# Performance work log

Measured on AMD Instinct MI355X. Metric: run time of the kernel, lower is better.

## Reference

```python
import jax, jax.numpy as jnp
import numpy as np

N = 4096        # nodes
D = 512         # in_dim = hidden_dim
E = 131072      # edges (avg degree 32)
K = 3           # aggregate_range
ALPHA = 2.0


def prelu(x, a):
    return jnp.where(x >= 0, x, a * x)


def setup_inputs() -> dict:
    key = jax.random.key(0)
    ks = jax.random.split(key, 8)
    s = 1.0 / np.sqrt(D)  # ~xavier scale
    return {
        "coeffs": jax.random.normal(ks[0], (N, D), jnp.float32),
        "edge_index": jax.random.randint(ks[1], (2, E), 0, N, dtype=jnp.int32),
        "W0": jax.random.normal(ks[2], (D, D), jnp.float32) * s,
        "b0": jnp.zeros((D,), jnp.float32),
        "a0": jnp.full((1,), 0.25, jnp.float32),
        "W1": jax.random.normal(ks[3], (D, D), jnp.float32) * s,  # use_bias=False
        "a1": jnp.full((1,), 0.25, jnp.float32),
        "W2": jax.random.normal(ks[4], (D, D), jnp.float32) * s,
        "a2": jnp.full((1,), 0.25, jnp.float32),
        "Wo": jax.random.normal(ks[5], (1, D), jnp.float32) * s,
        "bo": jnp.zeros((1,), jnp.float32),
    }


def _mlp(coeffs, W0, b0, a0, W1, a1, W2, a2, Wo, bo):
    # Linear+PReLU, then n_hidden_layers x [Linear(no bias)+PReLU+(Dropout: eval, no-op)], then Linear
    x = prelu(coeffs @ W0.T + b0, a0)
    x = prelu(x @ W1.T, a1)
    x = prelu(x @ W2.T, a2)
    return x @ Wo.T + bo  # [N, 1]


def _aggregate_k_hop(edge_index, angles):
    # Faithful to the torch code: enhanced_angles aliases angles, so each hop
    # reads the CURRENT (already enhanced) values:  a <- a + w_k * A_k @ a.
    # Hop 1 uses raw edge list (duplicate edges add twice). Hops >= 2 use
    # np.unique-deduplicated composed paths == boolean adjacency powers.
    src, dst = edge_index[0], edge_index[1]
    a = angles
    a = a + (0.5 ** ALPHA) * jax.ops.segment_sum(a[dst], src, num_segments=N)
    A = jnp.zeros((N, N), jnp.float32).at[src, dst].set(1.0)  # dedup'd boolean adjacency
    Ak = A
    for k_ in range(K - 1):
        Ak = ((Ak @ A) > 0).astype(jnp.float32)  # unique k-hop paths
        a = a + (1.0 / (k_ + 3)) ** ALPHA * (Ak @ a)
    return a


def reference(coeffs, edge_index, W0, b0, a0, W1, a1, W2, a2, Wo, bo):
    angles = _mlp(coeffs, W0, b0, a0, W1, a1, W2, a2, Wo, bo)
    return _aggregate_k_hop(edge_index, angles)
```

## Files before the change

kernel.cpp:

```cpp
#include <hip/hip_runtime.h>

#define N_NODES 4096
#define D_DIM   512
#define E_EDGES 131072
#define NWORDS  128
#define MLP_BLOCKS 256

typedef __bf16 bf16;
typedef __bf16 bf16x4 __attribute__((ext_vector_type(4)));
typedef __bf16 bf16x8 __attribute__((ext_vector_type(8)));
typedef float  f32x4  __attribute__((ext_vector_type(4)));
typedef unsigned int u32;

static const size_t OFF_W0P = 0;
static const size_t OFF_W1P = OFF_W0P + (size_t)D_DIM*D_DIM*2;
static const size_t OFF_W2P = OFF_W1P + (size_t)D_DIM*D_DIM*2;
static const size_t OFF_ANG = OFF_W2P + (size_t)D_DIM*D_DIM*2;
static const size_t OFF_H1  = OFF_ANG + N_NODES*4;
static const size_t OFF_A2V = OFF_H1  + N_NODES*4;
static const size_t OFF_TP  = OFF_A2V + N_NODES*4;
static const size_t OFF_AB  = OFF_TP  + 1024*4;
static const size_t OFF_A2B = OFF_AB  + (size_t)N_NODES*NWORDS*4;
static const size_t OFF_A3B = OFF_A2B + (size_t)N_NODES*NWORDS*4;

__device__ __forceinline__ bf16x8 cvt8(float4 lo, float4 hi) {
    bf16x8 r;
    r[0] = (bf16)lo.x; r[1] = (bf16)lo.y; r[2] = (bf16)lo.z; r[3] = (bf16)lo.w;
    r[4] = (bf16)hi.x; r[5] = (bf16)hi.y; r[6] = (bf16)hi.z; r[7] = (bf16)hi.w;
    return r;
}

__global__ __launch_bounds__(256)
void prep(const float* __restrict__ W0, const float* __restrict__ W1,
          const float* __restrict__ W2,
          bf16* __restrict__ W0p, bf16* __restrict__ W1p, bf16* __restrict__ W2p,
          u32* __restrict__ Ab, float* __restrict__ h1)
{
    const int bx = blockIdx.x, t = threadIdx.x;
    if (bx < 192) {
        const int layer = bx >> 6;
        const float* src = (layer == 0) ? W0 : (layer == 1) ? W1 : W2;
        bf16* dst = (layer == 0) ? W0p : (layer == 1) ? W1p : W2p;
        #pragma unroll
        for (int i = 0; i < 2; ++i) {
            int p = (bx & 63) * 512 + i * 256 + t;
            int colblk = p >> 12, ks = (p >> 8) & 15, f = (p >> 6) & 3, lane = p & 63;
            int col = colblk * 64 + f * 16 + (lane & 15);
            int k   = ks * 32 + (lane >> 4) * 8;
            const float* s = src + (size_t)col * D_DIM + k;
            float4 lo = *(const float4*)(s);
            float4 hi = *(const float4*)(s + 4);
            *(bf16x8*)(dst + (size_t)p * 8) = cvt8(lo, hi);
        }
    } else if (bx < 320) {
        uint4* dst = (uint4*)Ab + (size_t)(bx - 192) * 1024;
        uint4 z = {0u, 0u, 0u, 0u};
        #pragma unroll
        for (int i = 0; i < 4; ++i) dst[i * 256 + t] = z;
    } else {
        for (int i = t; i < N_NODES; i += 256) h1[i] = 0.f;
    }
}

__device__ __forceinline__ void gemm16x64(const bf16 (*xin)[512], const bf16* __restrict__ Wp,
                                          int wave, int lane, int lq, int quad, f32x4 acc[4])
{
    #pragma unroll
    for (int ks = 0; ks < 16; ++ks) {
        bf16x8 a = *(const bf16x8*)&xin[lq][(((ks * 4 + quad) ^ (lq & 7)) << 3)];
        #pragma unroll
        for (int f = 0; f < 4; ++f) {
            bf16x8 b = *(const bf16x8*)(Wp + ((size_t)((wave * 16 + ks) * 4 + f) * 64 + lane) * 8);
            acc[f] = __builtin_amdgcn_mfma_f32_16x16x32_bf16(a, b, acc[f], 0, 0, 0);
        }
    }
}

__device__ __forceinline__ void store_act(bf16 (*xout)[512], const f32x4 acc[4],
                                          int col0, int lq, int quad,
                                          const float* __restrict__ bias, float sl)
{
    #pragma unroll
    for (int f = 0; f < 4; ++f) {
        int col = col0 + f * 16 + lq;
        float bv = bias ? bias[col] : 0.f;
        int c = col >> 3, e = col & 7;
        #pragma unroll
        for (int r = 0; r < 4; ++r) {
            int row = quad * 4 + r;
            float v = acc[f][r] + bv;
            v = (v >= 0.f) ? v : sl * v;
            xout[row][((c ^ (row & 7)) << 3) + e] = (bf16)v;
        }
    }
}

__global__ __launch_bounds__(512)
void mlp_fused(const float* __restrict__ coeffs,
               const bf16* __restrict__ W0p, const bf16* __restrict__ W1p,
               const bf16* __restrict__ W2p,
               const float* __restrict__ b0, const float* __restrict__ pa0,
               const float* __restrict__ pa1, const float* __restrict__ pa2,
               const float* __restrict__ Wo, const float* __restrict__ bo,
               float* __restrict__ ang,
               const int* __restrict__ esrc, const int* __restrict__ edst,
               u32* __restrict__ AbOut)
{
    __shared__ bf16 xa[16][512];
    __shared__ bf16 xb[16][512];
    __shared__ float s_ang[8][16];
    const int bx = blockIdx.x, t = threadIdx.x;

    if (bx < MLP_BLOCKS) {
        const int wave = t >> 6, lane = t & 63;
        const int quad = lane >> 4, lq = lane & 15;
        const int rb = bx * 16;
        const int col0 = wave * 64;

        {
            int r = t >> 5;
            int kc = (t & 31) * 16;
            const float* src = coeffs + (size_t)(rb + r) * 512 + kc;
            float4 v0 = *(const float4*)(src);
            float4 v1 = *(const float4*)(src + 4);
            float4 v2 = *(const float4*)(src + 8);
            float4 v3 = *(const float4*)(src + 12);
            int c0 = kc >> 3;
            *(bf16x8*)&xa[r][((c0 ^ (r & 7)) << 3)]       = cvt8(v0, v1);
            *(bf16x8*)&xa[r][(((c0 + 1) ^ (r & 7)) << 3)] = cvt8(v2, v3);
        }
        __syncthreads();

        {
            f32x4 acc[4] = {};
            gemm16x64(xa, W0p, wave, lane, lq, quad, acc);
            store_act(xb, acc, col0, lq, quad, b0, pa0[0]);
        }
        __syncthreads();
        {
            f32x4 acc[4] = {};
            gemm16x64(xb, W1p, wave, lane, lq, quad, acc);
            store_act(xa, acc, col0, lq, quad, nullptr, pa1[0]);
        }
        __syncthreads();
        {
            f32x4 acc[4] = {};
            gemm16x64(xa, W2p, wave, lane, lq, quad, acc);
            const float sl = pa2[0];
            float wo[4];
            #pragma unroll
            for (int f = 0; f < 4; ++f) wo[f] = Wo[col0 + f * 16 + lq];
            #pragma unroll
            for (int r = 0; r < 4; ++r) {
                float p = 0.f;
                #pragma unroll
                for (int f = 0; f < 4; ++f) {
                    float v = acc[f][r];
                    v = (v >= 0.f) ? v : sl * v;
                    p += v * wo[f];
                }
                #pragma unroll
                for (int m = 1; m < 16; m <<= 1) p += __shfl_xor(p, m, 64);
                if (lq == 0) s_ang[wave][quad * 4 + r] = p;
            }
        }
        __syncthreads();
        if (t < 16) {
            float s = bo[0];
            #pragma unroll
            for (int w2 = 0; w2 < 8; ++w2) s += s_ang[w2][t];
            ang[rb + t] = s;
        }
    } else {
        int base = (bx - MLP_BLOCKS) * 512 + t;
        for (int e = base; e < E_EDGES; e += 128 * 512) {
            int r = esrc[e], c = edst[e];
            atomicOr(&AbOut[(size_t)r * NWORDS + (c >> 5)], 1u << (c & 31));
        }
    }
}

__device__ __forceinline__ void row_or(int row, int wave, int lane,
                                       int* s_cnt, int (*s_list)[256],
                                       const u32* __restrict__ P, const u32* __restrict__ Q,
                                       u32* __restrict__ BOut)
{
    if (lane == 0) s_cnt[wave] = 0;
    __syncthreads();
    const u32* prow = P + (size_t)row * NWORDS;
    #pragma unroll
    for (int h = 0; h < 2; ++h) {
        u32 bits = prow[h * 64 + lane];
        int base = (h * 64 + lane) * 32;
        while (bits) {
            int b = __ffs(bits) - 1; bits &= bits - 1;
            int pos = atomicAdd(&s_cnt[wave], 1);
            if (pos < 256) s_list[wave][pos] = base + b;
        }
    }
    __syncthreads();
    int cnt = min(s_cnt[wave], 256);
    u32 acc0 = 0, acc1 = 0;
    int j = 0;
    for (; j + 4 <= cnt; j += 4) {
        int i0 = s_list[wave][j], i1 = s_list[wave][j + 1];
        int i2 = s_list[wave][j + 2], i3 = s_list[wave][j + 3];
        const u32* q0 = Q + (size_t)i0 * NWORDS;
        const u32* q1 = Q + (size_t)i1 * NWORDS;
        const u32* q2 = Q + (size_t)i2 * NWORDS;
        const u32* q3 = Q + (size_t)i3 * NWORDS;
        u32 x0 = q0[lane], x1 = q1[lane], x2 = q2[lane], x3 = q3[lane];
        u32 y0 = q0[64 + lane], y1 = q1[64 + lane], y2 = q2[64 + lane], y3 = q3[64 + lane];
        acc0 |= x0 | x1 | x2 | x3;
        acc1 |= y0 | y1 | y2 | y3;
    }
    for (; j < cnt; ++j) {
        const u32* q = Q + (size_t)s_list[wave][j] * NWORDS;
        acc0 |= q[lane]; acc1 |= q[64 + lane];
    }
    BOut[(size_t)row * NWORDS + lane]      = acc0;
    BOut[(size_t)row * NWORDS + 64 + lane] = acc1;
}

__global__ __launch_bounds__(256)
void hop1_rowor(const int* __restrict__ src, const int* __restrict__ dst,
                const float* __restrict__ ang, float* __restrict__ h1,
                const u32* __restrict__ P, const u32* __restrict__ Q, u32* __restrict__ BOut)
{
    __shared__ int s_cnt[4];
    __shared__ int s_list[4][256];
    const int bx = blockIdx.x, t = threadIdx.x;
    const int wave = t >> 6, lane = t & 63;
    if (bx < 512) {
        int e = bx * 256 + t;
        atomicAdd(&h1[src[e]], 0.25f * ang[dst[e]]);
    } else {
        row_or((bx - 512) * 4 + wave, wave, lane, s_cnt, s_list, P, Q, BOut);
    }
}

__global__ __launch_bounds__(256)
void bmv2_rowor(const u32* __restrict__ A2, const float* __restrict__ ang,
                const float* __restrict__ h1, float* __restrict__ a2,
                float* __restrict__ Tpart,
                const u32* __restrict__ P, const u32* __restrict__ Q, u32* __restrict__ BOut)
{
    __shared__ float aLds[N_NODES];
    __shared__ float s_red[4];
    __shared__ int s_cnt[4];
    __shared__ int s_list[4][256];
    const int bx = blockIdx.x, t = threadIdx.x;
    const int wave = t >> 6, lane = t & 63;

    if (bx < 1024) {
        #pragma unroll
        for (int i = 0; i < 4; ++i) {
            int e = (i * 256 + t) * 4;
            float4 va = *(const float4*)(ang + e);
            float4 vh = *(const float4*)(h1 + e);
            float4 o; o.x = va.x + vh.x; o.y = va.y + vh.y; o.z = va.z + vh.z; o.w = va.w + vh.w;
            *(float4*)(aLds + e) = o;
        }
        __syncthreads();

        int row = bx * 4 + wave;
        float s = 0.f;
        #pragma unroll
        for (int h = 0; h < 2; ++h) {
            u32 bits = A2[(size_t)row * NWORDS + h * 64 + lane];
            int base = (h * 64 + lane) * 32;
            while (bits) {
                int b = __ffs(bits) - 1;
                bits &= bits - 1;
                s += aLds[base + b];
            }
        }
        #pragma unroll
        for (int off = 32; off > 0; off >>= 1) s += __shfl_down(s, off, 64);
        if (lane == 0) {
            float val = aLds[row] + (1.f / 9.f) * s;
            a2[row] = val;
            s_red[wave] = val;
        }
        __syncthreads();
        if (t == 0)
            Tpart[bx] = s_red[0] + s_red[1] + s_red[2] + s_red[3];
    } else {
        row_or((bx - 1024) * 4 + wave, wave, lane, s_cnt, s_list, P, Q, BOut);
    }
}

__global__ __launch_bounds__(256)
void bits_matvec3(const u32* __restrict__ A3, const float* __restrict__ a2,
                  const float* __restrict__ Tpart, float* __restrict__ out)
{
    __shared__ float aLds[N_NODES];
    __shared__ float s_part[4];
    const int t = threadIdx.x, wave = t >> 6, lane = t & 63;

    #pragma unroll
    for (int i = 0; i < 4; ++i) {
        int e = (i * 256 + t) * 4;
        *(float4*)(aLds + e) = *(const float4*)(a2 + e);
    }

    float tsum = 0.f;
    #pragma unroll
    for (int i = 0; i < 4; ++i) tsum += Tpart[i * 256 + t];
    #pragma unroll
    for (int off = 32; off > 0; off >>= 1) tsum += __shfl_down(tsum, off, 64);
    if (lane == 0) s_part[wave] = tsum;
    __syncthreads();
    const float T = s_part[0] + s_part[1] + s_part[2] + s_part[3];

    int row = blockIdx.x * 4 + wave;
    float s = 0.f;
    #pragma unroll
    for (int h = 0; h < 2; ++h) {
        u32 bits = ~A3[(size_t)row * NWORDS + h * 64 + lane];
        int base = (h * 64 + lane) * 32;
        while (bits) {
            int b = __ffs(bits) - 1;
            bits &= bits - 1;
            s += aLds[base + b];
        }
    }
    #pragma unroll
    for (int off = 32; off > 0; off >>= 1) s += __shfl_down(s, off, 64);
    if (lane == 0) out[row] = aLds[row] + (1.f / 16.f) * (T - s);
}

extern "C" void kernel_launch(void* const* d_in, const int* in_sizes, int n_in,
                              void* d_out, int out_size, void* d_ws, size_t ws_size,
                              hipStream_t stream) {
    const float* coeffs = (const float*)d_in[0];
    const int*   edges  = (const int*)d_in[1];
    const float* W0     = (const float*)d_in[2];
    const float* b0     = (const float*)d_in[3];
    const float* pa0    = (const float*)d_in[4];
    const float* W1     = (const float*)d_in[5];
    const float* pa1    = (const float*)d_in[6];
    const float* W2     = (const float*)d_in[7];
    const float* pa2    = (const float*)d_in[8];
    const float* Wo     = (const float*)d_in[9];
    const float* bo     = (const float*)d_in[10];
    float* out = (float*)d_out;

    char* ws = (char*)d_ws;
    bf16*  W0p  = (bf16*)(ws + OFF_W0P);
    bf16*  W1p  = (bf16*)(ws + OFF_W1P);
    bf16*  W2p  = (bf16*)(ws + OFF_W2P);
    float* ang  = (float*)(ws + OFF_ANG);
    float* h1   = (float*)(ws + OFF_H1);
    float* a2v  = (float*)(ws + OFF_A2V);
    float* Tp   = (float*)(ws + OFF_TP);
    u32*   Ab   = (u32*)(ws + OFF_AB);
    u32*   A2b  = (u32*)(ws + OFF_A2B);
    u32*   A3b  = (u32*)(ws + OFF_A3B);

    const int* srcp = edges;
    const int* dstp = edges + E_EDGES;

    prep<<<321, 256, 0, stream>>>(W0, W1, W2, W0p, W1p, W2p, Ab, h1);

    mlp_fused<<<MLP_BLOCKS + 128, 512, 0, stream>>>(coeffs, W0p, W1p, W2p, b0, pa0, pa1, pa2,
                                                    Wo, bo, ang, srcp, dstp, Ab);

    hop1_rowor<<<1536, 256, 0, stream>>>(srcp, dstp, ang, h1, Ab, Ab, A2b);

    bmv2_rowor<<<2048, 256, 0, stream>>>(A2b, ang, h1, a2v, Tp, Ab, A2b, A3b);

    bits_matvec3<<<1024, 256, 0, stream>>>(A3b, a2v, Tp, out);
}
```

Before: 129.7 us.

## Build adjacency bitmap in prep via per-block LDS row-range scans

Adjacency bitmap construction moves out of the MLP kernel's extra blocks into the prep kernel. Each of 128 blocks owns 32 rows, scans the full edge list, and sets bits with LDS atomicOr before one coalesced write to global memory. This removes the global zero-fill and the scattered global atomics, and frees the MLP kernel from sharing the GPU with the edge blocks. The cost is that every block reads all 131072 edge sources, about 128x redundant reads of esrc, which hit in L2 but add per-block loop latency.

After: 267.4 us. +106.2%, slower.

```diff
diff --git a/kernel.cpp b/kernel.cpp
--- a/kernel.cpp
+++ b/kernel.cpp
@@ -34,8 +34,10 @@
 void prep(const float* __restrict__ W0, const float* __restrict__ W1,
           const float* __restrict__ W2,
           bf16* __restrict__ W0p, bf16* __restrict__ W1p, bf16* __restrict__ W2p,
+          const int* __restrict__ esrc, const int* __restrict__ edst,
           u32* __restrict__ Ab, float* __restrict__ h1)
 {
+    __shared__ u32 sAb[32][NWORDS];
     const int bx = blockIdx.x, t = threadIdx.x;
     if (bx < 192) {
         const int layer = bx >> 6;
@@ -53,10 +55,23 @@
             *(bf16x8*)(dst + (size_t)p * 8) = cvt8(lo, hi);
         }
     } else if (bx < 320) {
-        uint4* dst = (uint4*)Ab + (size_t)(bx - 192) * 1024;
-        uint4 z = {0u, 0u, 0u, 0u};
-        #pragma unroll
-        for (int i = 0; i < 4; ++i) dst[i * 256 + t] = z;
+        int r0 = (bx - 192) * 32;
+        #pragma unroll
+        for (int i = 0; i < 16; ++i) ((u32*)sAb)[i * 256 + t] = 0u;
+        __syncthreads();
+        for (int e = t; e < E_EDGES; e += 256) {
+            int r = esrc[e];
+            if ((unsigned)(r - r0) < 32u) {
+                int c = edst[e];
+                atomicOr(&sAb[r - r0][c >> 5], 1u << (c & 31));
+            }
+        }
+        __syncthreads();
+        #pragma unroll
+        for (int i = 0; i < 16; ++i) {
+            int w = i * 256 + t;
+            Ab[(size_t)r0 * NWORDS + w] = ((u32*)sAb)[w];
+        }
     } else {
         for (int i = t; i < N_NODES; i += 256) h1[i] = 0.f;
     }
@@ -102,81 +117,71 @@
                const float* __restrict__ b0, const float* __restrict__ pa0,
                const float* __restrict__ pa1, const float* __restrict__ pa2,
                const float* __restrict__ Wo, const float* __restrict__ bo,
-               float* __restrict__ ang,
-               const int* __restrict__ esrc, const int* __restrict__ edst,
-               u32* __restrict__ AbOut)
+               float* __restrict__ ang)
 {
     __shared__ bf16 xa[16][512];
     __shared__ bf16 xb[16][512];
     __shared__ float s_ang[8][16];
     const int bx = blockIdx.x, t = threadIdx.x;
 
-    if (bx < MLP_BLOCKS) {
-        const int wave = t >> 6, lane = t & 63;
-        const int quad = lane >> 4, lq = lane & 15;
-        const int rb = bx * 16;
-        const int col0 = wave * 64;
-
-        {
-            int r = t >> 5;
-            int kc = (t & 31) * 16;
-            const float* src = coeffs + (size_t)(rb + r) * 512 + kc;
-            float4 v0 = *(const float4*)(src);
-            float4 v1 = *(const float4*)(src + 4);
-            float4 v2 = *(const float4*)(src + 8);
-            float4 v3 = *(const float4*)(src + 12);
-            int c0 = kc >> 3;
-            *(bf16x8*)&xa[r][((c0 ^ (r & 7)) << 3)]       = cvt8(v0, v1);
-            *(bf16x8*)&xa[r][(((c0 + 1) ^ (r & 7)) << 3)] = cvt8(v2, v3);
-        }
-        __syncthreads();
-
-        {
-            f32x4 acc[4] = {};
-            gemm16x64(xa, W0p, wave, lane, lq, quad, acc);
-            store_act(xb, acc, col0, lq, quad, b0, pa0[0]);
-        }
-        __syncthreads();
-        {
-            f32x4 acc[4] = {};
-            gemm16x64(xb, W1p, wave, lane, lq, quad, acc);
-            store_act(xa, acc, col0, lq, quad, nullptr, pa1[0]);
-        }
-        __syncthreads();
-        {
-            f32x4 acc[4] = {};
-            gemm16x64(xa, W2p, wave, lane, lq, quad, acc);
-            const float sl = pa2[0];
-            float wo[4];
+    const int wave = t >> 6, lane = t & 63;
+    const int quad = lane >> 4, lq = lane & 15;
+    const int rb = bx * 16;
+    const int col0 = wave * 64;
+
+    {
+        int r = t >> 5;
+        int kc = (t & 31) * 16;
+        const float* src = coeffs + (size_t)(rb + r) * 512 + kc;
+        float4 v0 = *(const float4*)(src);
+        float4 v1 = *(const float4*)(src + 4);
+        float4 v2 = *(const float4*)(src + 8);
+        float4 v3 = *(const float4*)(src + 12);
+        int c0 = kc >> 3;
+        *(bf16x8*)&xa[r][((c0 ^ (r & 7)) << 3)]       = cvt8(v0, v1);
+        *(bf16x8*)&xa[r][(((c0 + 1) ^ (r & 7)) << 3)] = cvt8(v2, v3);
+    }
+    __syncthreads();
+
+    {
+        f32x4 acc[4] = {};
+        gemm16x64(xa, W0p, wave, lane, lq, quad, acc);
+        store_act(xb, acc, col0, lq, quad, b0, pa0[0]);
+    }
+    __syncthreads();
+    {
+        f32x4 acc[4] = {};
+        gemm16x64(xb, W1p, wave, lane, lq, quad, acc);
+        store_act(xa, acc, col0, lq, quad, nullptr, pa1[0]);
+    }
+    __syncthreads();
+    {
+        f32x4 acc[4] = {};
+        gemm16x64(xa, W2p, wave, lane, lq, quad, acc);
+        const float sl = pa2[0];
+        float wo[4];
+        #pragma unroll
+        for (int f = 0; f < 4; ++f) wo[f] = Wo[col0 + f * 16 + lq];
+        #pragma unroll
+        for (int r = 0; r < 4; ++r) {
+            float p = 0.f;
             #pragma unroll
-            for (int f = 0; f < 4; ++f) wo[f] = Wo[col0 + f * 16 + lq];
+            for (int f = 0; f < 4; ++f) {
+                float v = acc[f][r];
+                v = (v >= 0.f) ? v : sl * v;
+                p += v * wo[f];
+            }
             #pragma unroll
-            for (int r = 0; r < 4; ++r) {
-                float p = 0.f;
-                #pragma unroll
-                for (int f = 0; f < 4; ++f) {
-                    float v = acc[f][r];
-                    v = (v >= 0.f) ? v : sl * v;
-                    p += v * wo[f];
-                }
-                #pragma unroll
-                for (int m = 1; m < 16; m <<= 1) p += __shfl_xor(p, m, 64);
-                if (lq == 0) s_ang[wave][quad * 4 + r] = p;
-            }
-        }
-        __syncthreads();
-        if (t < 16) {
-            float s = bo[0];
-            #pragma unroll
-            for (int w2 = 0; w2 < 8; ++w2) s += s_ang[w2][t];
-            ang[rb + t] = s;
-        }
-    } else {
-        int base = (bx - MLP_BLOCKS) * 512 + t;
-        for (int e = base; e < E_EDGES; e += 128 * 512) {
-            int r = esrc[e], c = edst[e];
-            atomicOr(&AbOut[(size_t)r * NWORDS + (c >> 5)], 1u << (c & 31));
-        }
+            for (int m = 1; m < 16; m <<= 1) p += __shfl_xor(p, m, 64);
+            if (lq == 0) s_ang[wave][quad * 4 + r] = p;
+        }
+    }
+    __syncthreads();
+    if (t < 16) {
+        float s = bo[0];
+        #pragma unroll
+        for (int w2 = 0; w2 < 8; ++w2) s += s_ang[w2][t];
+        ang[rb + t] = s;
     }
 }
 
@@ -361,10 +366,10 @@
     const int* srcp = edges;
     const int* dstp = edges + E_EDGES;
 
-    prep<<<321, 256, 0, stream>>>(W0, W1, W2, W0p, W1p, W2p, Ab, h1);
-
-    mlp_fused<<<MLP_BLOCKS + 128, 512, 0, stream>>>(coeffs, W0p, W1p, W2p, b0, pa0, pa1, pa2,
-                                                    Wo, bo, ang, srcp, dstp, Ab);
+    prep<<<321, 256, 0, stream>>>(W0, W1, W2, W0p, W1p, W2p, srcp, dstp, Ab, h1);
+
+    mlp_fused<<<MLP_BLOCKS, 512, 0, stream>>>(coeffs, W0p, W1p, W2p, b0, pa0, pa1, pa2,
+                                              Wo, bo, ang);
 
     hop1_rowor<<<1536, 256, 0, stream>>>(srcp, dstp, ang, h1, Ab, Ab, A2b);
 
```
